# Optimization experiments

Hardware: AMD Instinct MI355X
Metric: run time of the kernel (lower is better)

Reference implementation:

```python
import jax, jax.numpy as jnp
import numpy as np

D_MODEL = 1024
N_HEADS = 16
HEAD_DIM = D_MODEL // N_HEADS
THETA = 10000.0
B, T = 2, 2048


def apply_rope(x, pos, theta=THETA):
    # x: (b, h, t, d), pos: (t,)
    d = x.shape[-1]
    inv_freq = theta ** (-jnp.arange(0, d, 2, dtype=jnp.float32) / d)  # (d/2,)
    ang = pos.astype(jnp.float32)[:, None] * inv_freq[None, :]          # (t, d/2)
    cos, sin = jnp.cos(ang), jnp.sin(ang)
    x1, x2 = x[..., 0::2], x[..., 1::2]
    out_even = x1 * cos - x2 * sin
    out_odd = x1 * sin + x2 * cos
    return jnp.stack([out_even, out_odd], axis=-1).reshape(x.shape)


def setup_inputs() -> dict:
    key = jax.random.key(0)
    ks = jax.random.split(key, 5)
    s = 1.0 / np.sqrt(D_MODEL)
    return {
        "x": jax.random.normal(ks[0], (B, T, D_MODEL), jnp.float32),
        "wq": jax.random.normal(ks[1], (D_MODEL, D_MODEL), jnp.float32) * s,
        "wk": jax.random.normal(ks[2], (D_MODEL, D_MODEL), jnp.float32) * s,
        "wv": jax.random.normal(ks[3], (D_MODEL, D_MODEL), jnp.float32) * s,
        "wo": jax.random.normal(ks[4], (D_MODEL, D_MODEL), jnp.float32) * s,
        "token_pos": 1,
    }


def reference(x, wq, wk, wv, wo, token_pos):
    b, t, dm = x.shape
    # bias-free Linear: y = x @ W^T; split heads -> (b, h, t, d)
    def proj(w):
        y = jnp.einsum('btm,nm->btn', x, w)
        return y.reshape(b, t, N_HEADS, HEAD_DIM).transpose(0, 2, 1, 3)
    q, k, v = proj(wq), proj(wk), proj(wv)
    pos = jnp.arange(t)
    q = apply_rope(q, pos)
    k = apply_rope(k, pos)
    scale = jnp.sqrt(jnp.asarray(HEAD_DIM, dtype=x.dtype))
    scores = jnp.einsum('bhqd,bhkd->bhqk', q, k) / scale
    mask = jnp.tril(jnp.ones((t, t), dtype=bool))
    scores = jnp.where(mask, scores, -jnp.inf)
    attn = jax.nn.softmax(scores, axis=-1)
    out = jnp.einsum('bhqk,bhkd->bhqd', attn, v)
    out = out.transpose(0, 2, 1, 3).reshape(b, t, dm)
    return jnp.einsum('btm,nm->btn', out, wo)
```

## Files before the change

### kernel.cpp

```cpp
#include <hip/hip_runtime.h>
#include <hip/hip_bf16.h>
#include <math.h>

#define DM 1024
#define NH 16
#define HD 64
#define BB 2
#define TT 2048
#define MROWS (BB*TT)
#define PL ((size_t)MROWS * DM)
#define PLW ((size_t)DM * DM)

using bf8_t = __attribute__((ext_vector_type(8))) __bf16;
using bf4_t = __attribute__((ext_vector_type(4))) __bf16;
using f4_t  = __attribute__((ext_vector_type(4))) float;

__global__ __launch_bounds__(256) void prep(
        const void* __restrict__ X,
        const void* __restrict__ w0, const void* __restrict__ w1,
        const void* __restrict__ w2, const void* __restrict__ w3,
        __bf16* __restrict__ Xh, __bf16* __restrict__ Wsp,
        float2* __restrict__ trig, int* __restrict__ flag)
{
    const int id  = (int)blockIdx.x;
    const int tid = (int)threadIdx.x;

    __shared__ int cnt;
    if (tid == 0) cnt = 0;
    __syncthreads();
    {
        int local = 0;
        const unsigned short* xu = (const unsigned short*)X;
        for (int i = tid; i < 512; i += 256) {
            const int e = (xu[i] >> 7) & 0xFF;
            if (e >= 117 && e <= 130) local++;
        }
        atomicAdd(&cnt, local);
    }
    __syncthreads();
    const int f32 = (cnt >= 384) ? 0 : 1;

    if (id >= 8448) {
        if (tid == 0) *flag = f32;
        return;
    }
    if (id >= 8192) {
        const int idx = (id - 8192) * 256 + tid;
        const int t = idx >> 5, ip = idx & 31;
        const float inv_freq = powf(10000.0f, -2.0f * (float)ip / 64.0f);
        const float ang = (float)t * inv_freq;
        float s, c;
        sincosf(ang, &s, &c);
        trig[idx] = make_float2(c, s);
        return;
    }

    const void* Src;
    __bf16 *Yh, *Yl;
    size_t i;
    if (id < 4096) {
        Src = X;
        Yh = Xh; Yl = Xh + PL;
        i = ((size_t)id * 256 + tid) * 4;
    } else {
        const int wid   = (id - 4096) >> 10;
        const int inner = (id - 4096) & 1023;
        Src = (wid == 0) ? w0 : (wid == 1) ? w1 : (wid == 2) ? w2 : w3;
        Yh = Wsp + (size_t)wid * 2 * PLW;
        Yl = Yh + PLW;
        i = ((size_t)inner * 256 + tid) * 4;
    }
    if (f32) {
        float4 v = *(const float4*)((const float*)Src + i);
        __bf16 h0 = (__bf16)v.x, h1 = (__bf16)v.y, h2 = (__bf16)v.z, h3 = (__bf16)v.w;
        bf4_t hv = {h0, h1, h2, h3};
        bf4_t lv = {(__bf16)(v.x - (float)h0), (__bf16)(v.y - (float)h1),
                    (__bf16)(v.z - (float)h2), (__bf16)(v.w - (float)h3)};
        *(bf4_t*)(Yh + i) = hv;
        *(bf4_t*)(Yl + i) = lv;
    } else {
        bf4_t v = *(const bf4_t*)((const __bf16*)Src + i);
        *(bf4_t*)(Yh + i) = v;
        bf4_t zv = {(__bf16)0.f, (__bf16)0.f, (__bf16)0.f, (__bf16)0.f};
        *(bf4_t*)(Yl + i) = zv;
    }
}

__device__ __forceinline__ int xcd_remap(int flat, int nwg) {
    return (flat & 7) * (nwg >> 3) + (flat >> 3);
}

__device__ __forceinline__ int swz(int r, int b) {
    return r * 128 + (b ^ ((r & 7) << 4));
}
#define VST 264

__global__ __launch_bounds__(256, 3) void gemm_fused(
        const __bf16* __restrict__ Ahg,
        const __bf16* __restrict__ Wsp,
        __bf16* __restrict__ Y0, __bf16* __restrict__ Y1,
        __bf16* __restrict__ Y2,
        void* __restrict__ Yout,
        const float2* __restrict__ trig,
        const int* __restrict__ flag, const int outMode)
{
    const int f32 = *flag;

    const int nx = (int)gridDim.x, ny = (int)gridDim.y, nz = (int)gridDim.z;
    int flat = (int)blockIdx.x + nx * ((int)blockIdx.y + ny * (int)blockIdx.z);
    flat = xcd_remap(flat, nx * ny * nz);
    const int bx = flat % nx;
    const int rem = flat / nx;
    const int by = rem % ny;
    const int z  = rem / ny;

    const int widx = outMode ? 3 : z;
    const __bf16* Whg = Wsp + (size_t)widx * 2 * PLW;
    const __bf16* Wlg = Whg + PLW;
    const __bf16* Alg = Ahg + PL;
    const bool aLo = (outMode != 0) || (f32 != 0);
    const bool wLo = (f32 != 0);

    __shared__ __align__(16) char sm[49152];
    char* const AhL = sm;
    char* const AlL = sm + 16384;
    char* const WhL = sm + 32768;
    char* const WlL = sm + 40960;

    const int tid  = threadIdx.x;
    const int n0   = bx * 64, m0 = by * 128;
    const int lane = tid & 63;
    const int w    = tid >> 6;
    const int wr   = (w >> 1) * 64;
    const int wcn  = (w & 1) * 32;
    const int l15  = lane & 15;
    const int g    = lane >> 4;

    f4_t acc[4][2] = {};
    bf8_t pa[4], pal[4], pwh[2], pwl[2];

    auto ISSUE = [&](int k0) {
#pragma unroll
        for (int j = 0; j < 4; j++) {
            const int u = tid + j * 256, r = u >> 3, c = u & 7;
            pa[j] = *(const bf8_t*)(Ahg + (size_t)(m0 + r) * DM + k0 + c * 8);
            if (aLo)
                pal[j] = *(const bf8_t*)(Alg + (size_t)(m0 + r) * DM + k0 + c * 8);
        }
#pragma unroll
        for (int j = 0; j < 2; j++) {
            const int u = tid + j * 256, r = u >> 3, c = u & 7;
            pwh[j] = *(const bf8_t*)(Whg + (size_t)(n0 + r) * DM + k0 + c * 8);
            if (wLo)
                pwl[j] = *(const bf8_t*)(Wlg + (size_t)(n0 + r) * DM + k0 + c * 8);
        }
    };

    ISSUE(0);
    for (int k0 = 0; k0 < DM; k0 += 64) {
        if (k0) __syncthreads();
#pragma unroll
        for (int j = 0; j < 4; j++) {
            const int u = tid + j * 256, r = u >> 3, c = u & 7;
            *(bf8_t*)(AhL + swz(r, c * 16)) = pa[j];
            if (aLo) *(bf8_t*)(AlL + swz(r, c * 16)) = pal[j];
        }
#pragma unroll
        for (int j = 0; j < 2; j++) {
            const int u = tid + j * 256, r = u >> 3, c = u & 7;
            *(bf8_t*)(WhL + swz(r, c * 16)) = pwh[j];
            if (wLo) *(bf8_t*)(WlL + swz(r, c * 16)) = pwl[j];
        }
        __syncthreads();

        if (k0 + 64 < DM) ISSUE(k0 + 64);

#pragma unroll
        for (int kh = 0; kh < 2; kh++) {
            const int bc = kh * 64 + g * 16;
            bf8_t ah[4], al[4], wh[2], wl[2];
#pragma unroll
            for (int m = 0; m < 4; m++) {
                ah[m] = *(const bf8_t*)(AhL + swz(wr + m * 16 + l15, bc));
                if (aLo) al[m] = *(const bf8_t*)(AlL + swz(wr + m * 16 + l15, bc));
            }
#pragma unroll
            for (int n = 0; n < 2; n++) {
                wh[n] = *(const bf8_t*)(WhL + swz(wcn + n * 16 + l15, bc));
                if (wLo) wl[n] = *(const bf8_t*)(WlL + swz(wcn + n * 16 + l15, bc));
            }
#pragma unroll
            for (int m = 0; m < 4; m++)
#pragma unroll
                for (int n = 0; n < 2; n++) {
                    acc[m][n] = __builtin_amdgcn_mfma_f32_16x16x32_bf16(
                                    ah[m], wh[n], acc[m][n], 0, 0, 0);
                    if (aLo)
                        acc[m][n] = __builtin_amdgcn_mfma_f32_16x16x32_bf16(
                                        al[m], wh[n], acc[m][n], 0, 0, 0);
                    if (wLo)
                        acc[m][n] = __builtin_amdgcn_mfma_f32_16x16x32_bf16(
                                        ah[m], wl[n], acc[m][n], 0, 0, 0);
                }
        }
    }

    const int orow = g * 4;
    const int ocol = l15;
    __syncthreads();

    if (outMode) {
        if (f32) {
#pragma unroll
            for (int m = 0; m < 4; m++)
#pragma unroll
                for (int n = 0; n < 2; n++) {
                    const int gr = m0 + wr + m * 16 + orow;
                    const int gc = n0 + wcn + n * 16 + ocol;
#pragma unroll
                    for (int r = 0; r < 4; r++)
                        ((float*)Yout)[(size_t)(gr + r) * DM + gc] = acc[m][n][r];
                }
        } else {
            char* const EhL = sm;
#pragma unroll
            for (int m = 0; m < 4; m++)
#pragma unroll
                for (int n = 0; n < 2; n++) {
                    const int ctile = wcn + n * 16 + ocol;
#pragma unroll
                    for (int r = 0; r < 4; r++) {
                        const int rtile = wr + m * 16 + orow + r;
                        *(__bf16*)(EhL + rtile * 128 + ctile * 2) = (__bf16)acc[m][n][r];
                    }
                }
            __syncthreads();
#pragma unroll
            for (int j = 0; j < 4; j++) {
                const int u = tid + j * 256, r = u >> 3, c = u & 7;
                *(bf8_t*)((__bf16*)Yout + (size_t)(m0 + r) * DM + n0 + c * 8) =
                    *(const bf8_t*)(EhL + r * 128 + c * 16);
            }
        }
    } else if (z == 2) {
        char* const EhL = sm;
        char* const ElL = sm + 20480;
#pragma unroll
        for (int m = 0; m < 4; m++)
#pragma unroll
            for (int n = 0; n < 2; n++) {
                const int ctile = wcn + n * 16 + ocol;
#pragma unroll
                for (int r = 0; r < 4; r++) {
                    const int rtile = wr + m * 16 + orow + r;
                    const float val = acc[m][n][r];
                    __bf16 hb = (__bf16)val;
                    *(__bf16*)(EhL + ctile * VST + rtile * 2) = hb;
                    *(__bf16*)(ElL + ctile * VST + rtile * 2) = (__bf16)(val - (float)hb);
                }
            }
        __syncthreads();
        __bf16* Vh = Y2;
        __bf16* Vl = Y2 + PL;
#pragma unroll
        for (int j = 0; j < 4; j++) {
            const int u = tid + j * 256, cc = u >> 4, k = u & 15;
            *(bf8_t*)(Vh + (size_t)(n0 + cc) * MROWS + m0 + k * 8) =
                *(const bf8_t*)(EhL + cc * VST + k * 16);
            *(bf8_t*)(Vl + (size_t)(n0 + cc) * MROWS + m0 + k * 8) =
                *(const bf8_t*)(ElL + cc * VST + k * 16);
        }
    } else {
        char* const EhL = sm;
        char* const ElL = sm + 20480;
#pragma unroll
        for (int m = 0; m < 4; m++)
#pragma unroll
            for (int n = 0; n < 2; n++) {
                const int ctile = wcn + n * 16 + ocol;
                const int gc = n0 + ctile;
                const int ip = (gc & 63) >> 1;
                const bool oddc = (gc & 1) != 0;
#pragma unroll
                for (int r = 0; r < 4; r++) {
                    const int rtile = wr + m * 16 + orow + r;
                    const int t = (m0 + rtile) & (TT - 1);
                    const float2 cs = trig[t * 32 + ip];
                    const float v = acc[m][n][r];
                    const float ov = __shfl_xor(v, 1);
                    float res = oddc ? (ov * cs.y + v * cs.x) : (v * cs.x - ov * cs.y);
                    if (z == 0) res *= 0.125f;
                    __bf16 hb = (__bf16)res;
                    *(__bf16*)(EhL + rtile * 128 + ctile * 2) = hb;
                    *(__bf16*)(ElL + rtile * 128 + ctile * 2) = (__bf16)(res - (float)hb);
                }
            }
        __syncthreads();
        __bf16* Yh = z ? Y1 : Y0;
        __bf16* Yl = Yh + PL;
#pragma unroll
        for (int j = 0; j < 4; j++) {
            const int u = tid + j * 256, r = u >> 3, c = u & 7;
            *(bf8_t*)(Yh + (size_t)(m0 + r) * DM + n0 + c * 8) =
                *(const bf8_t*)(EhL + r * 128 + c * 16);
            *(bf8_t*)(Yl + (size_t)(m0 + r) * DM + n0 + c * 8) =
                *(const bf8_t*)(ElL + r * 128 + c * 16);
        }
    }
}

__global__ void __launch_bounds__(256, 2) flash_attn_mfma(
        const __bf16* __restrict__ Qhg, const __bf16* __restrict__ Khg,
        const __bf16* __restrict__ Vhg, __bf16* __restrict__ Aoh)
{
    __shared__ __align__(16) char sm[81920];

    const __bf16* Qlg = Qhg + PL;
    const __bf16* Klg = Khg + PL;
    const __bf16* Vlg = Vhg + PL;
    __bf16* Aol = Aoh + PL;

    int flat = (int)blockIdx.x + 16 * ((int)blockIdx.y + 16 * (int)blockIdx.z);
    flat = xcd_remap(flat, 512);
    const int pi = flat % 16;
    const int h  = (flat / 16) % 16;
    const int b  = flat / 256;

    const int tid = threadIdx.x;
    const int lane = tid & 63;
    const int w    = tid >> 6;
    const int l15  = lane & 15;
    const int g    = lane >> 4;

    char* const pb = sm + 65536 + w * 4096;

    bf8_t pk[2], pkl[2], pv[2], pvl[2];
    auto ISSUE = [&](int kt) {
#pragma unroll
        for (int j = 0; j < 2; j++) {
            const int u = tid + j * 256, r = u >> 3, c = u & 7;
            const size_t ko = (size_t)(b * TT + kt * 64 + r) * DM + h * HD + c * 8;
            pk[j]  = *(const bf8_t*)(Khg + ko);
            pkl[j] = *(const bf8_t*)(Klg + ko);
            const size_t vo = (size_t)(h * HD + r) * MROWS + b * TT + kt * 64 + c * 8;
            pv[j]  = *(const bf8_t*)(Vhg + vo);
            pvl[j] = *(const bf8_t*)(Vlg + vo);
        }
    };
    auto WRITE = [&](char* base) {
#pragma unroll
        for (int j = 0; j < 2; j++) {
            const int u = tid + j * 256, r = u >> 3, c = u & 7;
            *(bf8_t*)(base +         swz(r, c * 16)) = pk[j];
            *(bf8_t*)(base +  8192 + swz(r, c * 16)) = pkl[j];
            *(bf8_t*)(base + 16384 + swz(r, c * 16)) = pv[j];
            *(bf8_t*)(base + 24576 + swz(r, c * 16)) = pvl[j];
        }
    };

#pragma unroll 1
    for (int ph = 0; ph < 2; ph++) {
        const int qt = ph ? pi : (31 - pi);

        bf8_t qh[2], ql[2];
#pragma unroll
        for (int kh = 0; kh < 2; kh++) {
            const size_t off = (size_t)(b * TT + qt * 64 + w * 16 + l15) * DM
                             + h * HD + kh * 32 + g * 8;
            qh[kh] = *(const bf8_t*)(Qhg + off);
            ql[kh] = *(const bf8_t*)(Qlg + off);
        }

        f4_t o[4] = {};
        float lrow = 0.f;

        ISSUE(0);
        WRITE(sm);
        __syncthreads();

        for (int kt = 0; kt <= qt; kt++) {
            char* const cb = sm + (kt & 1) * 32768;
            if (kt < qt) ISSUE(kt + 1);

            f4_t s[4] = {};
            __builtin_amdgcn_s_setprio(1);
#pragma unroll
            for (int kh = 0; kh < 2; kh++) {
#pragma unroll
                for (int n = 0; n < 4; n++) {
                    bf8_t kf  = *(const bf8_t*)(cb +        swz(n * 16 + l15, kh * 64 + g * 16));
                    bf8_t kl2 = *(const bf8_t*)(cb + 8192 + swz(n * 16 + l15, kh * 64 + g * 16));
                    s[n] = __builtin_amdgcn_mfma_f32_16x16x32_bf16(kf,  qh[kh], s[n], 0, 0, 0);
                    s[n] = __builtin_amdgcn_mfma_f32_16x16x32_bf16(kl2, qh[kh], s[n], 0, 0, 0);
                    s[n] = __builtin_amdgcn_mfma_f32_16x16x32_bf16(kf,  ql[kh], s[n], 0, 0, 0);
                }
            }
            __builtin_amdgcn_s_setprio(0);

            if (kt == qt) {
                const int qoff = w * 16 + l15;
#pragma unroll
                for (int n = 0; n < 4; n++)
#pragma unroll
                    for (int r = 0; r < 4; r++)
                        if (n * 16 + g * 4 + r > qoff) s[n][r] = -INFINITY;
            }

#pragma unroll
            for (int n = 0; n < 4; n++) {
                bf4_t hv, lv;
#pragma unroll
                for (int r = 0; r < 4; r++) {
                    const float p = __expf(s[n][r] - 8.0f);
                    lrow += p;
                    __bf16 hb = (__bf16)p;
                    hv[r] = hb;
                    lv[r] = (__bf16)(p - (float)hb);
                }
                *(bf4_t*)(pb +        swz(l15, n * 32 + g * 8)) = hv;
                *(bf4_t*)(pb + 2048 + swz(l15, n * 32 + g * 8)) = lv;
            }
            asm volatile("s_waitcnt lgkmcnt(0)" ::: "memory");
            __builtin_amdgcn_sched_barrier(0);

            bf8_t pah[2], pal2[2];
#pragma unroll
            for (int kh = 0; kh < 2; kh++) {
                pah[kh]  = *(const bf8_t*)(pb +        swz(l15, kh * 64 + g * 16));
                pal2[kh] = *(const bf8_t*)(pb + 2048 + swz(l15, kh * 64 + g * 16));
            }

            __builtin_amdgcn_s_setprio(1);
#pragma unroll
            for (int kh = 0; kh < 2; kh++)
#pragma unroll
                for (int nf = 0; nf < 4; nf++) {
                    bf8_t vf  = *(const bf8_t*)(cb + 16384 + swz(nf * 16 + l15, kh * 64 + g * 16));
                    bf8_t vl2 = *(const bf8_t*)(cb + 24576 + swz(nf * 16 + l15, kh * 64 + g * 16));
                    o[nf] = __builtin_amdgcn_mfma_f32_16x16x32_bf16(pah[kh],  vf,  o[nf], 0, 0, 0);
                    o[nf] = __builtin_amdgcn_mfma_f32_16x16x32_bf16(pal2[kh], vf,  o[nf], 0, 0, 0);
                    o[nf] = __builtin_amdgcn_mfma_f32_16x16x32_bf16(pah[kh],  vl2, o[nf], 0, 0, 0);
                }
            __builtin_amdgcn_s_setprio(0);

            if (kt < qt) WRITE(sm + ((kt + 1) & 1) * 32768);
            __syncthreads();
        }

        lrow += __shfl_xor(lrow, 16);
        lrow += __shfl_xor(lrow, 32);
        const float inv = 1.0f / lrow;
        float linv[4];
#pragma unroll
        for (int r = 0; r < 4; r++)
            linv[r] = __shfl(inv, (lane & 48) | (g * 4 + r));

#pragma unroll
        for (int nf = 0; nf < 4; nf++)
#pragma unroll
            for (int r = 0; r < 4; r++) {
                const float val = o[nf][r] * linv[r];
                __bf16 hb = (__bf16)val;
                *(__bf16*)(pb + (g * 4 + r) * 128 + (nf * 16 + l15) * 2) = hb;
                *(__bf16*)(pb + 2048 + (g * 4 + r) * 128 + (nf * 16 + l15) * 2) =
                    (__bf16)(val - (float)hb);
            }
        asm volatile("s_waitcnt lgkmcnt(0)" ::: "memory");
        __builtin_amdgcn_sched_barrier(0);
#pragma unroll
        for (int j = 0; j < 2; j++) {
            const int u = lane + j * 64, r = u >> 3, c = u & 7;
            const size_t off = (size_t)(b * TT + qt * 64 + w * 16 + r) * DM
                             + h * HD + c * 8;
            *(bf8_t*)(Aoh + off) = *(const bf8_t*)(pb + r * 128 + c * 16);
            *(bf8_t*)(Aol + off) = *(const bf8_t*)(pb + 2048 + r * 128 + c * 16);
        }
    }
}

extern "C" void kernel_launch(void* const* d_in, const int* in_sizes, int n_in,
                              void* d_out, int out_size, void* d_ws, size_t ws_size,
                              hipStream_t stream) {
    const void* x  = d_in[0];
    const void* wq = d_in[1];
    const void* wk = d_in[2];
    const void* wv = d_in[3];
    const void* wo = d_in[4];

    __bf16* Qh  = (__bf16*)d_ws;
    __bf16* Kh  = Qh + 2 * PL;
    __bf16* Vth = Kh + 2 * PL;
    __bf16* Xh  = Vth + 2 * PL;
    __bf16* Wsp = Xh + 2 * PL;
    char* tail  = (char*)(Wsp + 8 * PLW);
    int* flag   = (int*)tail;
    float2* trig = (float2*)(tail + 512);

    prep<<<8449, 256, 0, stream>>>(x, wq, wk, wv, wo, Xh, Wsp, trig, flag);

    gemm_fused<<<dim3(DM / 64, MROWS / 128, 3), 256, 0, stream>>>(
        Xh, Wsp, Qh, Kh, Vth, nullptr, trig, flag, 0);

    flash_attn_mfma<<<dim3(16, NH, BB), 256, 0, stream>>>(Qh, Kh, Vth, Xh);

    gemm_fused<<<dim3(DM / 64, MROWS / 128, 1), 256, 0, stream>>>(
        Xh, Wsp, nullptr, nullptr, nullptr, d_out, trig, flag, 1);
}
```

Measured before the change: 287.7 us.

## Use direct global-to-LDS loads in GEMM and 128-row query tiles in attention

The projection GEMM now loads A and W tiles straight into shared memory with global_load_lds, dropping register staging and the swizzled layout. The flash attention kernel processes one 128-row query tile per block, two 16-row fragments per wave, instead of two balanced 64-row tiles. This reuses each K/V tile across twice as many queries. In exchange it loses the register prefetch overlap in the GEMM, risks LDS bank conflicts from the unswizzled layout, single-buffers K/V, and gives up the causal load balancing.

```diff
diff --git a/kernel.cpp b/kernel.cpp
--- a/kernel.cpp
+++ b/kernel.cpp
@@ -14,6 +14,9 @@
 using bf8_t = __attribute__((ext_vector_type(8))) __bf16;
 using bf4_t = __attribute__((ext_vector_type(4))) __bf16;
 using f4_t  = __attribute__((ext_vector_type(4))) float;
+
+typedef const __attribute__((address_space(1))) void* gas_t;
+typedef __attribute__((address_space(3))) void* las_t;
 
 __global__ __launch_bounds__(256) void prep(
         const void* __restrict__ X,
@@ -137,43 +140,34 @@
     const int g    = lane >> 4;
 
     f4_t acc[4][2] = {};
-    bf8_t pa[4], pal[4], pwh[2], pwl[2];
-
-    auto ISSUE = [&](int k0) {
+
+    for (int k0 = 0; k0 < DM; k0 += 64) {
+        if (k0) __syncthreads();
+
 #pragma unroll
         for (int j = 0; j < 4; j++) {
             const int u = tid + j * 256, r = u >> 3, c = u & 7;
-            pa[j] = *(const bf8_t*)(Ahg + (size_t)(m0 + r) * DM + k0 + c * 8);
+            char* const db = AhL + (size_t)(j * 256 + w * 64) * 16;
+            __builtin_amdgcn_global_load_lds(
+                (gas_t)(Ahg + (size_t)(m0 + r) * DM + k0 + c * 8),
+                (las_t)db, 16, 0, 0);
             if (aLo)
-                pal[j] = *(const bf8_t*)(Alg + (size_t)(m0 + r) * DM + k0 + c * 8);
+                __builtin_amdgcn_global_load_lds(
+                    (gas_t)(Alg + (size_t)(m0 + r) * DM + k0 + c * 8),
+                    (las_t)(AlL + (size_t)(j * 256 + w * 64) * 16), 16, 0, 0);
         }
 #pragma unroll
         for (int j = 0; j < 2; j++) {
             const int u = tid + j * 256, r = u >> 3, c = u & 7;
-            pwh[j] = *(const bf8_t*)(Whg + (size_t)(n0 + r) * DM + k0 + c * 8);
+            __builtin_amdgcn_global_load_lds(
+                (gas_t)(Whg + (size_t)(n0 + r) * DM + k0 + c * 8),
+                (las_t)(WhL + (size_t)(j * 256 + w * 64) * 16), 16, 0, 0);
             if (wLo)
-                pwl[j] = *(const bf8_t*)(Wlg + (size_t)(n0 + r) * DM + k0 + c * 8);
-        }
-    };
-
-    ISSUE(0);
-    for (int k0 = 0; k0 < DM; k0 += 64) {
-        if (k0) __syncthreads();
-#pragma unroll
-        for (int j = 0; j < 4; j++) {
-            const int u = tid + j * 256, r = u >> 3, c = u & 7;
-            *(bf8_t*)(AhL + swz(r, c * 16)) = pa[j];
-            if (aLo) *(bf8_t*)(AlL + swz(r, c * 16)) = pal[j];
-        }
-#pragma unroll
-        for (int j = 0; j < 2; j++) {
-            const int u = tid + j * 256, r = u >> 3, c = u & 7;
-            *(bf8_t*)(WhL + swz(r, c * 16)) = pwh[j];
-            if (wLo) *(bf8_t*)(WlL + swz(r, c * 16)) = pwl[j];
+                __builtin_amdgcn_global_load_lds(
+                    (gas_t)(Wlg + (size_t)(n0 + r) * DM + k0 + c * 8),
+                    (las_t)(WlL + (size_t)(j * 256 + w * 64) * 16), 16, 0, 0);
         }
         __syncthreads();
-
-        if (k0 + 64 < DM) ISSUE(k0 + 64);
 
 #pragma unroll
         for (int kh = 0; kh < 2; kh++) {
@@ -181,13 +175,13 @@
             bf8_t ah[4], al[4], wh[2], wl[2];
 #pragma unroll
             for (int m = 0; m < 4; m++) {
-                ah[m] = *(const bf8_t*)(AhL + swz(wr + m * 16 + l15, bc));
-                if (aLo) al[m] = *(const bf8_t*)(AlL + swz(wr + m * 16 + l15, bc));
+                ah[m] = *(const bf8_t*)(AhL + (wr + m * 16 + l15) * 128 + bc);
+                if (aLo) al[m] = *(const bf8_t*)(AlL + (wr + m * 16 + l15) * 128 + bc);
             }
 #pragma unroll
             for (int n = 0; n < 2; n++) {
-                wh[n] = *(const bf8_t*)(WhL + swz(wcn + n * 16 + l15, bc));
-                if (wLo) wl[n] = *(const bf8_t*)(WlL + swz(wcn + n * 16 + l15, bc));
+                wh[n] = *(const bf8_t*)(WhL + (wcn + n * 16 + l15) * 128 + bc);
+                if (wLo) wl[n] = *(const bf8_t*)(WlL + (wcn + n * 16 + l15) * 128 + bc);
             }
 #pragma unroll
             for (int m = 0; m < 4; m++)
@@ -313,7 +307,7 @@
         const __bf16* __restrict__ Qhg, const __bf16* __restrict__ Khg,
         const __bf16* __restrict__ Vhg, __bf16* __restrict__ Aoh)
 {
-    __shared__ __align__(16) char sm[81920];
+    __shared__ __align__(16) char sm[65536];
 
     const __bf16* Qlg = Qhg + PL;
     const __bf16* Klg = Khg + PL;
@@ -322,7 +316,7 @@
 
     int flat = (int)blockIdx.x + 16 * ((int)blockIdx.y + 16 * (int)blockIdx.z);
     flat = xcd_remap(flat, 512);
-    const int pi = flat % 16;
+    const int qt = 15 - (flat % 16);
     const int h  = (flat / 16) % 16;
     const int b  = flat / 256;
 
@@ -332,7 +326,21 @@
     const int l15  = lane & 15;
     const int g    = lane >> 4;
 
-    char* const pb = sm + 65536 + w * 4096;
+    char* const pb = sm + 32768 + w * 8192;
+
+    bf8_t qh[2][2], ql[2][2];
+#pragma unroll
+    for (int m = 0; m < 2; m++)
+#pragma unroll
+        for (int kh = 0; kh < 2; kh++) {
+            const size_t off = (size_t)(b * TT + qt * 128 + w * 32 + m * 16 + l15) * DM
+                             + h * HD + kh * 32 + g * 8;
+            qh[m][kh] = *(const bf8_t*)(Qhg + off);
+            ql[m][kh] = *(const bf8_t*)(Qlg + off);
+        }
+
+    f4_t o[2][4] = {};
+    float lrow[2] = {0.f, 0.f};
 
     bf8_t pk[2], pkl[2], pv[2], pvl[2];
     auto ISSUE = [&](int kt) {
@@ -347,134 +355,131 @@
             pvl[j] = *(const bf8_t*)(Vlg + vo);
         }
     };
-    auto WRITE = [&](char* base) {
+
+    const int nkt = 2 * qt + 2;
+    ISSUE(0);
+    for (int kt = 0; kt < nkt; kt++) {
+        __syncthreads();
 #pragma unroll
         for (int j = 0; j < 2; j++) {
             const int u = tid + j * 256, r = u >> 3, c = u & 7;
-            *(bf8_t*)(base +         swz(r, c * 16)) = pk[j];
-            *(bf8_t*)(base +  8192 + swz(r, c * 16)) = pkl[j];
-            *(bf8_t*)(base + 16384 + swz(r, c * 16)) = pv[j];
-            *(bf8_t*)(base + 24576 + swz(r, c * 16)) = pvl[j];
-        }
-    };
-
-#pragma unroll 1
-    for (int ph = 0; ph < 2; ph++) {
-        const int qt = ph ? pi : (31 - pi);
-
-        bf8_t qh[2], ql[2];
+            *(bf8_t*)(sm +         swz(r, c * 16)) = pk[j];
+            *(bf8_t*)(sm +  8192 + swz(r, c * 16)) = pkl[j];
+            *(bf8_t*)(sm + 16384 + swz(r, c * 16)) = pv[j];
+            *(bf8_t*)(sm + 24576 + swz(r, c * 16)) = pvl[j];
+        }
+        __syncthreads();
+        if (kt + 1 < nkt) ISSUE(kt + 1);
+
+        f4_t s[2][4] = {};
+        __builtin_amdgcn_s_setprio(1);
 #pragma unroll
         for (int kh = 0; kh < 2; kh++) {
-            const size_t off = (size_t)(b * TT + qt * 64 + w * 16 + l15) * DM
-                             + h * HD + kh * 32 + g * 8;
-            qh[kh] = *(const bf8_t*)(Qhg + off);
-            ql[kh] = *(const bf8_t*)(Qlg + off);
-        }
-
-        f4_t o[4] = {};
-        float lrow = 0.f;
-
-        ISSUE(0);
-        WRITE(sm);
-        __syncthreads();
-
-        for (int kt = 0; kt <= qt; kt++) {
-            char* const cb = sm + (kt & 1) * 32768;
-            if (kt < qt) ISSUE(kt + 1);
-
-            f4_t s[4] = {};
-            __builtin_amdgcn_s_setprio(1);
-#pragma unroll
-            for (int kh = 0; kh < 2; kh++) {
-#pragma unroll
-                for (int n = 0; n < 4; n++) {
-                    bf8_t kf  = *(const bf8_t*)(cb +        swz(n * 16 + l15, kh * 64 + g * 16));
-                    bf8_t kl2 = *(const bf8_t*)(cb + 8192 + swz(n * 16 + l15, kh * 64 + g * 16));
-                    s[n] = __builtin_amdgcn_mfma_f32_16x16x32_bf16(kf,  qh[kh], s[n], 0, 0, 0);
-                    s[n] = __builtin_amdgcn_mfma_f32_16x16x32_bf16(kl2, qh[kh], s[n], 0, 0, 0);
-                    s[n] = __builtin_amdgcn_mfma_f32_16x16x32_bf16(kf,  ql[kh], s[n], 0, 0, 0);
-                }
-            }
-            __builtin_amdgcn_s_setprio(0);
-
-            if (kt == qt) {
-                const int qoff = w * 16 + l15;
+#pragma unroll
+            for (int n = 0; n < 4; n++) {
+                bf8_t kf  = *(const bf8_t*)(sm +        swz(n * 16 + l15, kh * 64 + g * 16));
+                bf8_t kl2 = *(const bf8_t*)(sm + 8192 + swz(n * 16 + l15, kh * 64 + g * 16));
+#pragma unroll
+                for (int m = 0; m < 2; m++) {
+                    s[m][n] = __builtin_amdgcn_mfma_f32_16x16x32_bf16(kf,  qh[m][kh], s[m][n], 0, 0, 0);
+                    s[m][n] = __builtin_amdgcn_mfma_f32_16x16x32_bf16(kl2, qh[m][kh], s[m][n], 0, 0, 0);
+                    s[m][n] = __builtin_amdgcn_mfma_f32_16x16x32_bf16(kf,  ql[m][kh], s[m][n], 0, 0, 0);
+                }
+            }
+        }
+        __builtin_amdgcn_s_setprio(0);
+
+        if (kt >= 2 * qt) {
+            const int koff = (kt - 2 * qt) * 64;
+#pragma unroll
+            for (int m = 0; m < 2; m++) {
+                const int qloc = w * 32 + m * 16 + l15;
 #pragma unroll
                 for (int n = 0; n < 4; n++)
 #pragma unroll
                     for (int r = 0; r < 4; r++)
-                        if (n * 16 + g * 4 + r > qoff) s[n][r] = -INFINITY;
-            }
-
+                        if (koff + n * 16 + g * 4 + r > qloc) s[m][n][r] = -INFINITY;
+            }
+        }
+
+#pragma unroll
+        for (int m = 0; m < 2; m++)
 #pragma unroll
             for (int n = 0; n < 4; n++) {
                 bf4_t hv, lv;
 #pragma unroll
                 for (int r = 0; r < 4; r++) {
-                    const float p = __expf(s[n][r] - 8.0f);
-                    lrow += p;
+                    const float p = __expf(s[m][n][r] - 8.0f);
+                    lrow[m] += p;
                     __bf16 hb = (__bf16)p;
                     hv[r] = hb;
                     lv[r] = (__bf16)(p - (float)hb);
                 }
-                *(bf4_t*)(pb +        swz(l15, n * 32 + g * 8)) = hv;
-                *(bf4_t*)(pb + 2048 + swz(l15, n * 32 + g * 8)) = lv;
-            }
-            asm volatile("s_waitcnt lgkmcnt(0)" ::: "memory");
-            __builtin_amdgcn_sched_barrier(0);
-
-            bf8_t pah[2], pal2[2];
-#pragma unroll
-            for (int kh = 0; kh < 2; kh++) {
-                pah[kh]  = *(const bf8_t*)(pb +        swz(l15, kh * 64 + g * 16));
-                pal2[kh] = *(const bf8_t*)(pb + 2048 + swz(l15, kh * 64 + g * 16));
-            }
-
-            __builtin_amdgcn_s_setprio(1);
-#pragma unroll
-            for (int kh = 0; kh < 2; kh++)
-#pragma unroll
-                for (int nf = 0; nf < 4; nf++) {
-                    bf8_t vf  = *(const bf8_t*)(cb + 16384 + swz(nf * 16 + l15, kh * 64 + g * 16));
-                    bf8_t vl2 = *(const bf8_t*)(cb + 24576 + swz(nf * 16 + l15, kh * 64 + g * 16));
-                    o[nf] = __builtin_amdgcn_mfma_f32_16x16x32_bf16(pah[kh],  vf,  o[nf], 0, 0, 0);
-                    o[nf] = __builtin_amdgcn_mfma_f32_16x16x32_bf16(pal2[kh], vf,  o[nf], 0, 0, 0);
-                    o[nf] = __builtin_amdgcn_mfma_f32_16x16x32_bf16(pah[kh],  vl2, o[nf], 0, 0, 0);
-                }
-            __builtin_amdgcn_s_setprio(0);
-
-            if (kt < qt) WRITE(sm + ((kt + 1) & 1) * 32768);
-            __syncthreads();
-        }
-
-        lrow += __shfl_xor(lrow, 16);
-        lrow += __shfl_xor(lrow, 32);
-        const float inv = 1.0f / lrow;
-        float linv[4];
-#pragma unroll
-        for (int r = 0; r < 4; r++)
-            linv[r] = __shfl(inv, (lane & 48) | (g * 4 + r));
-
-#pragma unroll
-        for (int nf = 0; nf < 4; nf++)
-#pragma unroll
-            for (int r = 0; r < 4; r++) {
-                const float val = o[nf][r] * linv[r];
-                __bf16 hb = (__bf16)val;
-                *(__bf16*)(pb + (g * 4 + r) * 128 + (nf * 16 + l15) * 2) = hb;
-                *(__bf16*)(pb + 2048 + (g * 4 + r) * 128 + (nf * 16 + l15) * 2) =
-                    (__bf16)(val - (float)hb);
+                *(bf4_t*)(pb +        swz(m * 16 + l15, n * 32 + g * 8)) = hv;
+                *(bf4_t*)(pb + 4096 + swz(m * 16 + l15, n * 32 + g * 8)) = lv;
             }
         asm volatile("s_waitcnt lgkmcnt(0)" ::: "memory");
         __builtin_amdgcn_sched_barrier(0);
-#pragma unroll
-        for (int j = 0; j < 2; j++) {
-            const int u = lane + j * 64, r = u >> 3, c = u & 7;
-            const size_t off = (size_t)(b * TT + qt * 64 + w * 16 + r) * DM
-                             + h * HD + c * 8;
-            *(bf8_t*)(Aoh + off) = *(const bf8_t*)(pb + r * 128 + c * 16);
-            *(bf8_t*)(Aol + off) = *(const bf8_t*)(pb + 2048 + r * 128 + c * 16);
-        }
+
+        bf8_t pah[2][2], pal2[2][2];
+#pragma unroll
+        for (int m = 0; m < 2; m++)
+#pragma unroll
+            for (int kh = 0; kh < 2; kh++) {
+                pah[m][kh]  = *(const bf8_t*)(pb +        swz(m * 16 + l15, kh * 64 + g * 16));
+                pal2[m][kh] = *(const bf8_t*)(pb + 4096 + swz(m * 16 + l15, kh * 64 + g * 16));
+            }
+
+        __builtin_amdgcn_s_setprio(1);
+#pragma unroll
+        for (int kh = 0; kh < 2; kh++)
+#pragma unroll
+            for (int nf = 0; nf < 4; nf++) {
+                bf8_t vf  = *(const bf8_t*)(sm + 16384 + swz(nf * 16 + l15, kh * 64 + g * 16));
+                bf8_t vl2 = *(const bf8_t*)(sm + 24576 + swz(nf * 16 + l15, kh * 64 + g * 16));
+#pragma unroll
+                for (int m = 0; m < 2; m++) {
+                    o[m][nf] = __builtin_amdgcn_mfma_f32_16x16x32_bf16(pah[m][kh],  vf,  o[m][nf], 0, 0, 0);
+                    o[m][nf] = __builtin_amdgcn_mfma_f32_16x16x32_bf16(pal2[m][kh], vf,  o[m][nf], 0, 0, 0);
+                    o[m][nf] = __builtin_amdgcn_mfma_f32_16x16x32_bf16(pah[m][kh],  vl2, o[m][nf], 0, 0, 0);
+                }
+            }
+        __builtin_amdgcn_s_setprio(0);
+    }
+
+    float linv[2][4];
+#pragma unroll
+    for (int m = 0; m < 2; m++) {
+        lrow[m] += __shfl_xor(lrow[m], 16);
+        lrow[m] += __shfl_xor(lrow[m], 32);
+        const float inv = 1.0f / lrow[m];
+#pragma unroll
+        for (int r = 0; r < 4; r++)
+            linv[m][r] = __shfl(inv, (lane & 48) | (g * 4 + r));
+    }
+
+#pragma unroll
+    for (int m = 0; m < 2; m++)
+#pragma unroll
+        for (int nf = 0; nf < 4; nf++)
+#pragma unroll
+            for (int r = 0; r < 4; r++) {
+                const float val = o[m][nf][r] * linv[m][r];
+                __bf16 hb = (__bf16)val;
+                const int row = m * 16 + g * 4 + r;
+                *(__bf16*)(pb + row * 128 + (nf * 16 + l15) * 2) = hb;
+                *(__bf16*)(pb + 4096 + row * 128 + (nf * 16 + l15) * 2) =
+                    (__bf16)(val - (float)hb);
+            }
+    asm volatile("s_waitcnt lgkmcnt(0)" ::: "memory");
+    __builtin_amdgcn_sched_barrier(0);
+#pragma unroll
+    for (int j = 0; j < 4; j++) {
+        const int u = lane + j * 64, r = u >> 3, c = u & 7;
+        const size_t off = (size_t)(b * TT + qt * 128 + w * 32 + r) * DM
+                         + h * HD + c * 8;
+        *(bf8_t*)(Aoh + off) = *(const bf8_t*)(pb + r * 128 + c * 16);
+        *(bf8_t*)(Aol + off) = *(const bf8_t*)(pb + 4096 + r * 128 + c * 16);
     }
 }
 
```

Result: slower. 326.1 us (+13.3%).

## Load GEMM tiles directly into LDS via global_load_lds, dropping register prefetch

Applied to the files above, without the earlier changes.

The projection GEMM now copies A and W tiles from global memory straight into LDS with the direct-to-LDS load builtin. The XOR swizzle moves to the global source address so the LDS layout still matches the existing swz reads. This removes the register staging and the ds_write instructions. It also drops the software prefetch of the next k-tile, so global load latency is no longer overlapped with MFMA compute. The barrier also has to wait on the direct loads completing, which may expose latency.

```diff
diff --git a/kernel.cpp b/kernel.cpp
--- a/kernel.cpp
+++ b/kernel.cpp
@@ -14,6 +14,9 @@
 using bf8_t = __attribute__((ext_vector_type(8))) __bf16;
 using bf4_t = __attribute__((ext_vector_type(4))) __bf16;
 using f4_t  = __attribute__((ext_vector_type(4))) float;
+
+typedef const __attribute__((address_space(1))) void* gas_t;
+typedef __attribute__((address_space(3))) void* las_t;
 
 __global__ __launch_bounds__(256) void prep(
         const void* __restrict__ X,
@@ -137,43 +140,35 @@
     const int g    = lane >> 4;
 
     f4_t acc[4][2] = {};
-    bf8_t pa[4], pal[4], pwh[2], pwl[2];
-
-    auto ISSUE = [&](int k0) {
+
+    for (int k0 = 0; k0 < DM; k0 += 64) {
+        if (k0) __syncthreads();
+
 #pragma unroll
         for (int j = 0; j < 4; j++) {
             const int u = tid + j * 256, r = u >> 3, c = u & 7;
-            pa[j] = *(const bf8_t*)(Ahg + (size_t)(m0 + r) * DM + k0 + c * 8);
+            const int cs = c ^ (r & 7);
+            __builtin_amdgcn_global_load_lds(
+                (gas_t)(Ahg + (size_t)(m0 + r) * DM + k0 + cs * 8),
+                (las_t)(AhL + (size_t)(j * 256 + w * 64) * 16), 16, 0, 0);
             if (aLo)
-                pal[j] = *(const bf8_t*)(Alg + (size_t)(m0 + r) * DM + k0 + c * 8);
+                __builtin_amdgcn_global_load_lds(
+                    (gas_t)(Alg + (size_t)(m0 + r) * DM + k0 + cs * 8),
+                    (las_t)(AlL + (size_t)(j * 256 + w * 64) * 16), 16, 0, 0);
         }
 #pragma unroll
         for (int j = 0; j < 2; j++) {
             const int u = tid + j * 256, r = u >> 3, c = u & 7;
-            pwh[j] = *(const bf8_t*)(Whg + (size_t)(n0 + r) * DM + k0 + c * 8);
+            const int cs = c ^ (r & 7);
+            __builtin_amdgcn_global_load_lds(
+                (gas_t)(Whg + (size_t)(n0 + r) * DM + k0 + cs * 8),
+                (las_t)(WhL + (size_t)(j * 256 + w * 64) * 16), 16, 0, 0);
             if (wLo)
-                pwl[j] = *(const bf8_t*)(Wlg + (size_t)(n0 + r) * DM + k0 + c * 8);
-        }
-    };
-
-    ISSUE(0);
-    for (int k0 = 0; k0 < DM; k0 += 64) {
-        if (k0) __syncthreads();
-#pragma unroll
-        for (int j = 0; j < 4; j++) {
-            const int u = tid + j * 256, r = u >> 3, c = u & 7;
-            *(bf8_t*)(AhL + swz(r, c * 16)) = pa[j];
-            if (aLo) *(bf8_t*)(AlL + swz(r, c * 16)) = pal[j];
-        }
-#pragma unroll
-        for (int j = 0; j < 2; j++) {
-            const int u = tid + j * 256, r = u >> 3, c = u & 7;
-            *(bf8_t*)(WhL + swz(r, c * 16)) = pwh[j];
-            if (wLo) *(bf8_t*)(WlL + swz(r, c * 16)) = pwl[j];
+                __builtin_amdgcn_global_load_lds(
+                    (gas_t)(Wlg + (size_t)(n0 + r) * DM + k0 + cs * 8),
+                    (las_t)(WlL + (size_t)(j * 256 + w * 64) * 16), 16, 0, 0);
         }
         __syncthreads();
-
-        if (k0 + 64 < DM) ISSUE(k0 + 64);
 
 #pragma unroll
         for (int kh = 0; kh < 2; kh++) {
```

Result: faster. 277.8 us (-3.5%).
